# Performance work log

Hardware: AMD Instinct MI355X
Metric: run time of the kernel (lower is better)

Reference implementation:

```python
import math
import jax, jax.numpy as jnp
import numpy as np

# ---- hyperparams (match init_kwargs) ----
N_LEVELS = 16
F = 2                      # n_features_per_level
LOG2_T = 19                # log2_hashmap_size
BASE_RES = 16
PER_LEVEL_SCALE = 1.5
N_POINTS = 2 ** 21


def _aligned_level_size(res):
    return min(((res * res + 7) // 8) * 8, 1 << LOG2_T)

# static per-level resolution / offset tables (Python ints, mirror torch __init__)
RES, OFFS = [], []
_off = 0
_log2s = math.log2(PER_LEVEL_SCALE)
for _l in range(N_LEVELS):
    _scale = 2.0 ** (_l * _log2s) * BASE_RES - 1.0
    _r = int(math.ceil(_scale) + 1)
    RES.append(_r)
    OFFS.append(_off)
    _off += _aligned_level_size(_r)
TOTAL = _off
SIZES = [(OFFS[l + 1] - OFFS[l]) if l + 1 < N_LEVELS else TOTAL - OFFS[l]
         for l in range(N_LEVELS)]


def setup_inputs() -> dict:
    key = jax.random.key(0)
    k1, k2 = jax.random.split(key)
    # scale to [0, 0.95) so all 4 corner indices stay in-range on dense levels
    xy = jax.random.uniform(k1, (N_POINTS, 2), jnp.float32) * 0.95
    params = jax.random.uniform(k2, (TOTAL * F,), jnp.float32,
                                minval=-1e-4, maxval=1e-4)
    return {"xy": xy, "params": params}


def _grid_index(gx, gy, res, hsize):
    if hsize >= res * res:            # dense level
        return gx + gy * res
    # coherent prime hash in uint32 arithmetic (wraps == & 0xFFFFFFFF)
    h = (gx.astype(jnp.uint32) ^ (gy.astype(jnp.uint32) * jnp.uint32(2654435761)))
    return (h % jnp.uint32(hsize)).astype(jnp.int32)


def reference(xy, params):
    table = params.reshape(TOTAL, F)          # [TOTAL, F]
    outs = []
    for l in range(N_LEVELS):                 # small static loop over levels
        res, off, hsize = RES[l], OFFS[l], SIZES[l]
        pos = xy * (res - 1.0) + 0.5          # [N, 2]
        pg = jnp.floor(pos)
        frac = pos - pg
        pg = pg.astype(jnp.int32)
        gx0, gy0 = pg[:, 0], pg[:, 1]
        gx1, gy1 = gx0 + 1, gy0 + 1
        wx, wy = frac[:, 0:1], frac[:, 1:2]   # [N, 1]
        i00 = off + _grid_index(gx0, gy0, res, hsize)
        i10 = off + _grid_index(gx1, gy0, res, hsize)
        i01 = off + _grid_index(gx0, gy1, res, hsize)
        i11 = off + _grid_index(gx1, gy1, res, hsize)
        f00 = jnp.take(table, i00, axis=0)    # [N, F]
        f10 = jnp.take(table, i10, axis=0)
        f01 = jnp.take(table, i01, axis=0)
        f11 = jnp.take(table, i11, axis=0)
        out_l = (f00 * ((1.0 - wx) * (1.0 - wy))
                 + f10 * (wx * (1.0 - wy))
                 + f01 * ((1.0 - wx) * wy)
                 + f11 * (wx * wy))
        outs.append(out_l)
    return jnp.concatenate(outs, axis=-1)     # [N, N_LEVELS * F]
```

## Files before the change

kernel.cpp:

```cpp
#include <hip/hip_runtime.h>
#include <math.h>

#define N_LEVELS 16
#define NPTS (1 << 21)

typedef float vfloat4 __attribute__((ext_vector_type(4)));

struct LevelP {
    float scale;
    int   res;
    int   off;
    unsigned int mask;
    int   is_hash;
};
struct LevelTable { LevelP lv[N_LEVELS]; };

__global__ __launch_bounds__(256) void hashenc_kernel(
        const float2* __restrict__ xy,
        const float*  __restrict__ table,
        float4* __restrict__ out,
        LevelTable lt)
{
    int tid  = blockIdx.x * 256 + threadIdx.x;
    int pair = tid & 7;
    int p    = tid >> 3;

    float2 pt = xy[p];
    float4 o;

    #pragma unroll
    for (int k = 0; k < 2; ++k) {
        const LevelP lp = lt.lv[2 * pair + k];

        float px = __fadd_rn(__fmul_rn(pt.x, lp.scale), 0.5f);
        float py = __fadd_rn(__fmul_rn(pt.y, lp.scale), 0.5f);
        float fx = floorf(px), fy = floorf(py);
        float wx = __fsub_rn(px, fx), wy = __fsub_rn(py, fy);
        int gx = (int)fx, gy = (int)fy;

        int i00, i10, i01, i11;
        if (lp.is_hash) {
            const unsigned K1 = 2654435761u;
            unsigned ux = (unsigned)gx, uy = (unsigned)gy;
            unsigned hy0 = uy * K1, hy1 = (uy + 1u) * K1;
            i00 = (int)((ux        ^ hy0) & lp.mask);
            i10 = (int)(((ux + 1u) ^ hy0) & lp.mask);
            i01 = (int)((ux        ^ hy1) & lp.mask);
            i11 = (int)(((ux + 1u) ^ hy1) & lp.mask);
        } else {
            i00 = gx + gy * lp.res;
            i10 = i00 + 1;
            i01 = i00 + lp.res;
            i11 = i01 + 1;
        }

        const float2* tb = (const float2*)table + lp.off;
        float2 f00 = tb[i00];
        float2 f10 = tb[i10];
        float2 f01 = tb[i01];
        float2 f11 = tb[i11];

        float owx = 1.0f - wx, owy = 1.0f - wy;
        float w00 = owx * owy, w10 = wx * owy, w01 = owx * wy, w11 = wx * wy;
        float ox = f00.x * w00 + f10.x * w10 + f01.x * w01 + f11.x * w11;
        float oy = f00.y * w00 + f10.y * w10 + f01.y * w01 + f11.y * w11;

        if (k == 0) { o.x = ox; o.y = oy; }
        else        { o.z = ox; o.w = oy; }
    }

    vfloat4 ov = { o.x, o.y, o.z, o.w };
    __builtin_nontemporal_store(ov, (vfloat4*)&out[(size_t)p * 8 + pair]);
}

extern "C" void kernel_launch(void* const* d_in, const int* in_sizes, int n_in,
                              void* d_out, int out_size, void* d_ws, size_t ws_size,
                              hipStream_t stream) {
    const float2* xy     = (const float2*)d_in[0];
    const float*  params = (const float*)d_in[1];
    float4*       out    = (float4*)d_out;

    LevelTable lt;
    double log2s = log2(1.5);
    long offs[N_LEVELS];
    int  res_arr[N_LEVELS];
    long off = 0;
    for (int l = 0; l < N_LEVELS; ++l) {
        double scale = pow(2.0, (double)l * log2s) * 16.0 - 1.0;
        int r = (int)ceil(scale) + 1;
        res_arr[l] = r;
        offs[l] = off;
        long sz = ((long)r * r + 7) / 8 * 8;
        if (sz > (1L << 19)) sz = 1L << 19;
        off += sz;
    }
    for (int l = 0; l < N_LEVELS; ++l) {
        long hsize = ((l + 1 < N_LEVELS) ? offs[l + 1] : off) - offs[l];
        long r2 = (long)res_arr[l] * res_arr[l];
        int is_hash = hsize < r2;
        lt.lv[l].scale   = (float)(res_arr[l] - 1);
        lt.lv[l].res     = res_arr[l];
        lt.lv[l].off     = (int)offs[l];
        lt.lv[l].is_hash = is_hash;
        lt.lv[l].mask    = is_hash ? (unsigned)(hsize - 1) : 0u;
    }

    long total_threads = (long)NPTS * 8;
    dim3 grid((unsigned)(total_threads / 256)), block(256);
    hipLaunchKernelGGL(hashenc_kernel, grid, block, 0, stream,
                       xy, params, out, lt);
}
```

Before: 847.6 us.

## Split encoding per level with XCD-aware level mapping and separate interleave pass

Restructures the work so that each block handles a single level for 2048 points and writes planar per-level results to workspace. Levels are mapped onto XCDs, assuming round-robin block dispatch, so each XCD's L2 holds at most two hash tables. This is meant to cut L2 misses on the random table gathers. A second kernel then interleaves the planar buffers into the output layout, which costs an extra write and read of the full 256 MB output plus a second launch. The fused kernel is kept as a fallback when the workspace is too small.

```diff
diff --git a/kernel.cpp b/kernel.cpp
--- a/kernel.cpp
+++ b/kernel.cpp
@@ -5,6 +5,7 @@
 #define NPTS (1 << 21)
 
 typedef float vfloat4 __attribute__((ext_vector_type(4)));
+typedef float vfloat2 __attribute__((ext_vector_type(2)));
 
 struct LevelP {
     float scale;
@@ -14,23 +15,29 @@
     int   is_hash;
 };
 struct LevelTable { LevelP lv[N_LEVELS]; };
-
-__global__ __launch_bounds__(256) void hashenc_kernel(
+struct LevelMap   { int m[8][2]; };
+
+__global__ __launch_bounds__(256) void enc_level_kernel(
         const float2* __restrict__ xy,
         const float*  __restrict__ table,
-        float4* __restrict__ out,
-        LevelTable lt)
+        float2* __restrict__ ws,
+        LevelTable lt, LevelMap lm)
 {
-    int tid  = blockIdx.x * 256 + threadIdx.x;
-    int pair = tid & 7;
-    int p    = tid >> 3;
-
-    float2 pt = xy[p];
-    float4 o;
+    int xcd   = blockIdx.x & 7;
+    int slot  = blockIdx.x >> 3;
+    int lvl   = lm.m[xcd][slot >> 10];
+    int chunk = slot & 1023;
+
+    const LevelP lp = lt.lv[lvl];
+    const float2* tb = (const float2*)table + lp.off;
+    float2* wsl = ws + (size_t)lvl * NPTS;
+
+    int base = chunk * 2048 + threadIdx.x;
 
     #pragma unroll
-    for (int k = 0; k < 2; ++k) {
-        const LevelP lp = lt.lv[2 * pair + k];
+    for (int i = 0; i < 8; ++i) {
+        int p = base + i * 256;
+        float2 pt = xy[p];
 
         float px = __fadd_rn(__fmul_rn(pt.x, lp.scale), 0.5f);
         float py = __fadd_rn(__fmul_rn(pt.y, lp.scale), 0.5f);
@@ -54,6 +61,76 @@
             i11 = i01 + 1;
         }
 
+        float2 f00 = tb[i00];
+        float2 f10 = tb[i10];
+        float2 f01 = tb[i01];
+        float2 f11 = tb[i11];
+
+        float owx = 1.0f - wx, owy = 1.0f - wy;
+        float w00 = owx * owy, w10 = wx * owy, w01 = owx * wy, w11 = wx * wy;
+        vfloat2 o;
+        o.x = f00.x * w00 + f10.x * w10 + f01.x * w01 + f11.x * w11;
+        o.y = f00.y * w00 + f10.y * w10 + f01.y * w01 + f11.y * w11;
+
+        __builtin_nontemporal_store(o, (vfloat2*)&wsl[p]);
+    }
+}
+
+__global__ __launch_bounds__(256) void interleave_kernel(
+        const float2* __restrict__ ws,
+        float4* __restrict__ out)
+{
+    int tid  = blockIdx.x * 256 + threadIdx.x;
+    int pair = tid & 7;
+    int p    = tid >> 3;
+
+    const vfloat2* a = (const vfloat2*)(ws + (size_t)(2 * pair)     * NPTS);
+    const vfloat2* b = (const vfloat2*)(ws + (size_t)(2 * pair + 1) * NPTS);
+    vfloat2 va = __builtin_nontemporal_load(&a[p]);
+    vfloat2 vb = __builtin_nontemporal_load(&b[p]);
+
+    vfloat4 o = { va.x, va.y, vb.x, vb.y };
+    __builtin_nontemporal_store(o, (vfloat4*)&out[(size_t)p * 8 + pair]);
+}
+
+__global__ __launch_bounds__(256) void hashenc_kernel(
+        const float2* __restrict__ xy,
+        const float*  __restrict__ table,
+        float4* __restrict__ out,
+        LevelTable lt)
+{
+    int tid  = blockIdx.x * 256 + threadIdx.x;
+    int pair = tid & 7;
+    int p    = tid >> 3;
+
+    float2 pt = xy[p];
+    float4 o;
+
+    #pragma unroll
+    for (int k = 0; k < 2; ++k) {
+        const LevelP lp = lt.lv[2 * pair + k];
+        float px = __fadd_rn(__fmul_rn(pt.x, lp.scale), 0.5f);
+        float py = __fadd_rn(__fmul_rn(pt.y, lp.scale), 0.5f);
+        float fx = floorf(px), fy = floorf(py);
+        float wx = __fsub_rn(px, fx), wy = __fsub_rn(py, fy);
+        int gx = (int)fx, gy = (int)fy;
+
+        int i00, i10, i01, i11;
+        if (lp.is_hash) {
+            const unsigned K1 = 2654435761u;
+            unsigned ux = (unsigned)gx, uy = (unsigned)gy;
+            unsigned hy0 = uy * K1, hy1 = (uy + 1u) * K1;
+            i00 = (int)((ux        ^ hy0) & lp.mask);
+            i10 = (int)(((ux + 1u) ^ hy0) & lp.mask);
+            i01 = (int)((ux        ^ hy1) & lp.mask);
+            i11 = (int)(((ux + 1u) ^ hy1) & lp.mask);
+        } else {
+            i00 = gx + gy * lp.res;
+            i10 = i00 + 1;
+            i01 = i00 + lp.res;
+            i11 = i01 + 1;
+        }
+
         const float2* tb = (const float2*)table + lp.off;
         float2 f00 = tb[i00];
         float2 f10 = tb[i10];
@@ -105,8 +182,23 @@
         lt.lv[l].mask    = is_hash ? (unsigned)(hsize - 1) : 0u;
     }
 
-    long total_threads = (long)NPTS * 8;
-    dim3 grid((unsigned)(total_threads / 256)), block(256);
-    hipLaunchKernelGGL(hashenc_kernel, grid, block, 0, stream,
-                       xy, params, out, lt);
-}
+    size_t ws_needed = (size_t)N_LEVELS * NPTS * 2 * sizeof(float);
+    if (ws_size >= ws_needed) {
+        LevelMap lm;
+        int map[8][2] = { {10,0},{11,1},{12,2},{13,3},{14,4},{15,5},{6,7},{8,9} };
+        for (int x = 0; x < 8; ++x) { lm.m[x][0] = map[x][0]; lm.m[x][1] = map[x][1]; }
+
+        float2* ws = (float2*)d_ws;
+        dim3 gridA(16384), block(256);
+        hipLaunchKernelGGL(enc_level_kernel, gridA, block, 0, stream,
+                           xy, params, ws, lt, lm);
+        dim3 gridB((NPTS * 8) / 256);
+        hipLaunchKernelGGL(interleave_kernel, gridB, block, 0, stream,
+                           (const float2*)ws, out);
+    } else {
+        long total_threads = (long)NPTS * 8;
+        dim3 grid((unsigned)(total_threads / 256)), block(256);
+        hipLaunchKernelGGL(hashenc_kernel, grid, block, 0, stream,
+                           xy, params, out, lt);
+    }
+}
```

Result: faster. 771.7 us (-8.9%).
